# Kernel tuning notes

Measured on AMD Instinct MI355X. Metric: run time of the kernel, lower is better.

## Reference

```python
import jax, jax.numpy as jnp
import numpy as np

NT, NC, D = 20000, 80000, 256
SLOPE = 0.01  # torch F.leaky_relu default negative_slope


def _lrelu(x):
    return jnp.where(x >= 0, x, SLOPE * x)


def setup_inputs() -> dict:
    key = jax.random.key(0)
    ks = jax.random.split(key, 20)
    sc = 1.0 / np.sqrt(D)

    def W(k):
        return jax.random.normal(k, (D, D), jnp.float32) * sc

    return {
        "feat_table": jax.random.normal(ks[0], (NT, D), jnp.float32),
        "feat_column": jax.random.normal(ks[1], (NC, D), jnp.float32),
        "W_t2c": W(ks[2]), "b_t2c": jnp.zeros((D,), jnp.float32),
        "W_c2t": W(ks[3]), "b_c2t": jnp.zeros((D,), jnp.float32),
        "W_c2c": W(ks[4]), "b_c2c": jnp.zeros((D,), jnp.float32),
        "W_t2t": W(ks[5]), "b_t2t": jnp.zeros((D,), jnp.float32),
        "W_h": W(ks[6]), "b_h": jnp.zeros((D,), jnp.float32),
        "src_t2c": jax.random.randint(ks[7], (320000,), 0, NT, jnp.int32),
        "dst_t2c": jax.random.randint(ks[8], (320000,), 0, NC, jnp.int32),
        "src_c2t": jax.random.randint(ks[9], (320000,), 0, NC, jnp.int32),
        "dst_c2t": jax.random.randint(ks[10], (320000,), 0, NT, jnp.int32),
        "src_c2c": jax.random.randint(ks[11], (640000,), 0, NC, jnp.int32),
        "dst_c2c": jax.random.randint(ks[12], (640000,), 0, NC, jnp.int32),
        "src_t2t": jax.random.randint(ks[13], (160000,), 0, NT, jnp.int32),
        "dst_t2t": jax.random.randint(ks[14], (160000,), 0, NT, jnp.int32),
    }


def _mean_agg(Wh, src, dst, n_dst):
    # copy_u + mean: gather src messages, segment-mean into dst nodes
    s = jax.ops.segment_sum(Wh[src], dst, num_segments=n_dst)  # [n_dst, D]
    c = jax.ops.segment_sum(jnp.ones(src.shape, Wh.dtype), dst, num_segments=n_dst)
    return s / jnp.maximum(c, 1.0)[:, None]


def reference(feat_table, feat_column,
              W_t2c, b_t2c, W_c2t, b_c2t, W_c2c, b_c2c, W_t2t, b_t2t,
              W_h, b_h,
              src_t2c, dst_t2c, src_c2t, dst_c2t,
              src_c2c, dst_c2c, src_t2t, dst_t2t):
    # per-etype Linear + leaky_relu on source-node features
    Wh_t2c = _lrelu(feat_table @ W_t2c.T + b_t2c)
    Wh_c2t = _lrelu(feat_column @ W_c2t.T + b_c2t)
    Wh_c2c = _lrelu(feat_column @ W_c2c.T + b_c2c)
    Wh_t2t = _lrelu(feat_table @ W_t2t.T + b_t2t)

    # per-etype mean aggregation, then cross-etype 'mean' (2 etypes per ntype)
    h_table = 0.5 * (_mean_agg(Wh_c2t, src_c2t, dst_c2t, NT)
                     + _mean_agg(Wh_t2t, src_t2t, dst_t2t, NT))
    h_column = 0.5 * (_mean_agg(Wh_t2c, src_t2c, dst_t2c, NC)
                      + _mean_agg(Wh_c2c, src_c2c, dst_c2c, NC))

    out_table = _lrelu(h_table @ W_h.T + b_h) + feat_table
    out_column = _lrelu(h_column @ W_h.T + b_h) + feat_column
    return out_table, out_column
```

## Files before the change

kernel.cpp:

```cpp
#include <hip/hip_runtime.h>

#define D 256
#define SLOPE 0.01f

#define BSH 9
#define BSZ 512
#define NBMAX 160
#define EPB 8192

typedef __attribute__((ext_vector_type(8))) short bf16x8;
typedef __attribute__((ext_vector_type(4))) float f32x4;

__device__ __forceinline__ float bfbits2f(unsigned int hi) {
  return __builtin_bit_cast(float, hi);
}
__device__ __forceinline__ unsigned short f2bf(float f) {
  unsigned u = __builtin_bit_cast(unsigned, f);
  u += 0x7fffu + ((u >> 16) & 1u);
  return (unsigned short)(u >> 16);
}
__device__ __forceinline__ float lrelu(float x) {
  return (x >= 0.f) ? x : SLOPE * x;
}

__device__ __forceinline__ void gld_lds16(const void* g, void* l) {
  __builtin_amdgcn_global_load_lds(
      (const __attribute__((address_space(1))) unsigned int*)g,
      (__attribute__((address_space(3))) unsigned int*)l, 16, 0, 0);
}

__global__ void cast5_kernel(const float* w0, const float* w1, const float* w2,
                             const float* w3, const float* w4,
                             unsigned short* o0, unsigned short* o1,
                             unsigned short* o2, unsigned short* o3,
                             unsigned short* o4) {
  int a = blockIdx.y;
  const float* in = a == 0 ? w0 : a == 1 ? w1 : a == 2 ? w2 : a == 3 ? w3 : w4;
  unsigned short* out = a == 0 ? o0 : a == 1 ? o1 : a == 2 ? o2 : a == 3 ? o3 : o4;
  int i = blockIdx.x * blockDim.x + threadIdx.x;
  float4 v = ((const float4*)in)[i];
  ushort4 o;
  o.x = f2bf(v.x); o.y = f2bf(v.y); o.z = f2bf(v.z); o.w = f2bf(v.w);
  ((ushort4*)out)[i] = o;
}

__global__ __launch_bounds__(512, 1) void gemm0_dual(
    const float* __restrict__ Af, const unsigned short* __restrict__ B1,
    const unsigned short* __restrict__ B2, const float* __restrict__ bias1,
    const float* __restrict__ bias2, unsigned short* __restrict__ o1,
    unsigned short* __restrict__ o2, int M) {
  __shared__ __attribute__((aligned(16))) unsigned short Xs[64 * 256];
  const int t = threadIdx.x;
  const int wv = t >> 6, lane = t & 63;
  const int half = wv >> 2;
  const int w = wv & 3;
  const int mblk = blockIdx.x * 64;
  const int fr = lane & 15;
  const int jb = lane >> 4;

  const unsigned short* B = half ? B2 : B1;
  const float* bias = half ? bias2 : bias1;
  unsigned short* outb = half ? o2 : o1;

  float4 v0[4], v1[4];
  int cds[4];
#pragma unroll
  for (int i = 0; i < 4; i++) {
    const int c = i * 512 + t;
    const int m = c >> 5, jg = c & 31;
    int row = mblk + m;
    if (row > M - 1) row = M - 1;
    const float* gp = Af + (size_t)row * D + jg * 8;
    v0[i] = *(const float4*)gp;
    v1[i] = *(const float4*)(gp + 4);
    cds[i] = m * 32 + (jg ^ (m & 7));
  }

  bf16x8 wf[4][8];
  {
    const unsigned short* wp = B + (size_t)(w * 64 + fr) * D + jb * 8;
#pragma unroll
    for (int nt = 0; nt < 4; nt++)
#pragma unroll
      for (int k0 = 0; k0 < 8; k0++)
        wf[nt][k0] = *(const bf16x8*)(wp + nt * 16 * D + k0 * 32);
  }

#pragma unroll
  for (int i = 0; i < 4; i++) {
    uint4 pk;
    pk.x = (unsigned)f2bf(v0[i].x) | ((unsigned)f2bf(v0[i].y) << 16);
    pk.y = (unsigned)f2bf(v0[i].z) | ((unsigned)f2bf(v0[i].w) << 16);
    pk.z = (unsigned)f2bf(v1[i].x) | ((unsigned)f2bf(v1[i].y) << 16);
    pk.w = (unsigned)f2bf(v1[i].z) | ((unsigned)f2bf(v1[i].w) << 16);
    *(uint4*)&Xs[cds[i] * 8] = pk;
  }
  __syncthreads();

  f32x4 acc[4][4];
#pragma unroll
  for (int i = 0; i < 4; i++)
#pragma unroll
    for (int j = 0; j < 4; j++) acc[i][j] = (f32x4){0.f, 0.f, 0.f, 0.f};

  const int r = fr & 7;
#pragma unroll
  for (int k0 = 0; k0 < 8; k0++) {
    bf16x8 xf[4];
#pragma unroll
    for (int mt = 0; mt < 4; mt++) {
      const int ml = mt * 16 + fr;
      xf[mt] = *(const bf16x8*)&Xs[ml * 256 + (((k0 * 4 + jb) ^ r) * 8)];
    }
#pragma unroll
    for (int mt = 0; mt < 4; mt++)
#pragma unroll
      for (int nt = 0; nt < 4; nt++)
        acc[mt][nt] = __builtin_amdgcn_mfma_f32_16x16x32_bf16(
            wf[nt][k0], xf[mt], acc[mt][nt], 0, 0, 0);
  }

  const int n0 = w * 64 + jb * 4;
  float4 bv[4];
#pragma unroll
  for (int nt = 0; nt < 4; nt++) bv[nt] = *(const float4*)&bias[n0 + nt * 16];

#pragma unroll
  for (int mt = 0; mt < 4; mt++) {
    const int m = mblk + mt * 16 + fr;
    if (m < M) {
#pragma unroll
      for (int nt = 0; nt < 4; nt++) {
        ushort4 o;
        o.x = f2bf(lrelu(acc[mt][nt][0] + bv[nt].x));
        o.y = f2bf(lrelu(acc[mt][nt][1] + bv[nt].y));
        o.z = f2bf(lrelu(acc[mt][nt][2] + bv[nt].z));
        o.w = f2bf(lrelu(acc[mt][nt][3] + bv[nt].w));
        *(ushort4*)&outb[(size_t)m * D + n0 + nt * 16] = o;
      }
    }
  }
}

template <int MODE>
__global__ __launch_bounds__(256, 2) void gemm_v2(
    const unsigned short* __restrict__ A, const unsigned short* __restrict__ B,
    const float* __restrict__ bias, const float* __restrict__ residual,
    unsigned short* __restrict__ outb, float* __restrict__ outf, int M) {
  __shared__ __attribute__((aligned(16))) unsigned short Xs[64 * 256];
  const int t = threadIdx.x;
  const int w = t >> 6, lane = t & 63;
  const int mblk = blockIdx.x * 64;
  const int fr = lane & 15;
  const int jb = lane >> 4;

  bf16x8 wf[4][8];
  {
    const unsigned short* wp = B + (size_t)(w * 64 + fr) * D + jb * 8;
#pragma unroll
    for (int nt = 0; nt < 4; nt++)
#pragma unroll
      for (int k0 = 0; k0 < 8; k0++)
        wf[nt][k0] = *(const bf16x8*)(wp + nt * 16 * D + k0 * 32);
  }

#pragma unroll
  for (int i = 0; i < 8; i++) {
    const int m = (i * 4 + w) * 2 + (lane >> 5);
    int row = mblk + m;
    if (row > M - 1) row = M - 1;
    const int jsrc = (lane & 31) ^ (m & 7);
    gld_lds16(A + (size_t)row * D + jsrc * 8, &Xs[(i * 4 + w) * 512]);
  }
  asm volatile("s_waitcnt vmcnt(0)" ::: "memory");
  __syncthreads();

  f32x4 acc[4][4];
#pragma unroll
  for (int i = 0; i < 4; i++)
#pragma unroll
    for (int j = 0; j < 4; j++) acc[i][j] = (f32x4){0.f, 0.f, 0.f, 0.f};

  const int r = fr & 7;
#pragma unroll
  for (int k0 = 0; k0 < 8; k0++) {
    bf16x8 xf[4];
#pragma unroll
    for (int mt = 0; mt < 4; mt++) {
      const int ml = mt * 16 + fr;
      xf[mt] = *(const bf16x8*)&Xs[ml * 256 + (((k0 * 4 + jb) ^ r) * 8)];
    }
#pragma unroll
    for (int mt = 0; mt < 4; mt++)
#pragma unroll
      for (int nt = 0; nt < 4; nt++)
        acc[mt][nt] = __builtin_amdgcn_mfma_f32_16x16x32_bf16(
            wf[nt][k0], xf[mt], acc[mt][nt], 0, 0, 0);
  }

  const int n0 = w * 64 + jb * 4;
  float4 bv[4];
#pragma unroll
  for (int nt = 0; nt < 4; nt++) bv[nt] = *(const float4*)&bias[n0 + nt * 16];

#pragma unroll
  for (int mt = 0; mt < 4; mt++) {
    const int m = mblk + mt * 16 + fr;
    if (m < M) {
      if (MODE == 1) {
        float4 rv[4];
#pragma unroll
        for (int nt = 0; nt < 4; nt++)
          rv[nt] = *(const float4*)&residual[(size_t)m * D + n0 + nt * 16];
#pragma unroll
        for (int nt = 0; nt < 4; nt++) {
          float4 o;
          o.x = lrelu(acc[mt][nt][0] + bv[nt].x) + rv[nt].x;
          o.y = lrelu(acc[mt][nt][1] + bv[nt].y) + rv[nt].y;
          o.z = lrelu(acc[mt][nt][2] + bv[nt].z) + rv[nt].z;
          o.w = lrelu(acc[mt][nt][3] + bv[nt].w) + rv[nt].w;
          *(float4*)&outf[(size_t)m * D + n0 + nt * 16] = o;
        }
      } else {
#pragma unroll
        for (int nt = 0; nt < 4; nt++) {
          ushort4 o;
          o.x = f2bf(lrelu(acc[mt][nt][0] + bv[nt].x));
          o.y = f2bf(lrelu(acc[mt][nt][1] + bv[nt].y));
          o.z = f2bf(lrelu(acc[mt][nt][2] + bv[nt].z));
          o.w = f2bf(lrelu(acc[mt][nt][3] + bv[nt].w));
          *(ushort4*)&outb[(size_t)m * D + n0 + nt * 16] = o;
        }
      }
    }
  }
}

__global__ void hist4_kernel(const int* d0, int n0, int* c0, const int* d1,
                             int n1, int* c1, const int* d2, int n2, int* c2,
                             const int* d3, int n3, int* c3) {
  int a = blockIdx.y;
  const int* dst = a == 0 ? d0 : a == 1 ? d1 : a == 2 ? d2 : d3;
  int n = a == 0 ? n0 : a == 1 ? n1 : a == 2 ? n2 : n3;
  int* cnt = a == 0 ? c0 : a == 1 ? c1 : a == 2 ? c2 : c3;
  int i = blockIdx.x * blockDim.x + threadIdx.x;
  if (i < n) atomicAdd(&cnt[dst[i]], 1);
}

__global__ __launch_bounds__(256) void scan_p1(
    const int* c0, int n0, const int* c1, int n1, const int* c2, int n2,
    const int* c3, int n3, int* __restrict__ bsum) {
  int a = blockIdx.y;
  const int* cnt = a == 0 ? c0 : a == 1 ? c1 : a == 2 ? c2 : c3;
  int n = a == 0 ? n0 : a == 1 ? n1 : a == 2 ? n2 : n3;
  int nblk = (n + 1023) >> 10;
  int blk = blockIdx.x;
  if (blk >= nblk) return;
  int t = threadIdx.x;
  int i = (blk << 10) + t * 4;
  int s = 0;
  if (i + 3 < n) {
    int4 v = *(const int4*)(cnt + i);
    s = v.x + v.y + v.z + v.w;
  } else {
#pragma unroll
    for (int j = 0; j < 4; j++)
      if (i + j < n) s += cnt[i + j];
  }
  __shared__ int red[256];
  red[t] = s;
  __syncthreads();
  for (int off = 128; off > 0; off >>= 1) {
    if (t < off) red[t] += red[t + off];
    __syncthreads();
  }
  if (t == 0) bsum[a * 128 + blk] = red[0];
}

__global__ __launch_bounds__(128) void scan_p2(int* __restrict__ bsum, int* o0,
                                               int n0, int* o1, int n1, int* o2,
                                               int n2, int* o3, int n3) {
  int a = blockIdx.x;
  int* offs = a == 0 ? o0 : a == 1 ? o1 : a == 2 ? o2 : o3;
  int n = a == 0 ? n0 : a == 1 ? n1 : a == 2 ? n2 : n3;
  int nblk = (n + 1023) >> 10;
  int t = threadIdx.x;
  int v = (t < nblk) ? bsum[a * 128 + t] : 0;
  __shared__ int s[128];
  s[t] = v;
  __syncthreads();
  for (int off = 1; off < 128; off <<= 1) {
    int u = (t >= off) ? s[t - off] : 0;
    __syncthreads();
    s[t] += u;
    __syncthreads();
  }
  if (t < nblk) bsum[a * 128 + t] = s[t] - v;
  if (t == 127) offs[n] = s[127];
}

__global__ __launch_bounds__(256) void scan_p3(
    const int* c0, int* o0, int n0, const int* c1, int* o1, int n1,
    const int* c2, int* o2, int n2, const int* c3, int* o3, int n3,
    const int* __restrict__ bsum) {
  int a = blockIdx.y;
  const int* cnt = a == 0 ? c0 : a == 1 ? c1 : a == 2 ? c2 : c3;
  int* offs = a == 0 ? o0 : a == 1 ? o1 : a == 2 ? o2 : o3;
  int n = a == 0 ? n0 : a == 1 ? n1 : a == 2 ? n2 : n3;
  int nblk = (n + 1023) >> 10;
  int blk = blockIdx.x;
  if (blk >= nblk) return;
  int t = threadIdx.x;
  int i = (blk << 10) + t * 4;
  int4 v = {0, 0, 0, 0};
  if (i + 3 < n) {
    v = *(const int4*)(cnt + i);
  } else {
    if (i < n) v.x = cnt[i];
    if (i + 1 < n) v.y = cnt[i + 1];
    if (i + 2 < n) v.z = cnt[i + 2];
    if (i + 3 < n) v.w = cnt[i + 3];
  }
  int s = v.x + v.y + v.z + v.w;
  __shared__ int sm[256];
  sm[t] = s;
  __syncthreads();
  for (int off = 1; off < 256; off <<= 1) {
    int u = (t >= off) ? sm[t - off] : 0;
    __syncthreads();
    sm[t] += u;
    __syncthreads();
  }
  int ex = sm[t] - s + bsum[a * 128 + blk];
  int4 o;
  o.x = ex;
  o.y = ex + v.x;
  o.z = ex + v.x + v.y;
  o.w = ex + v.x + v.y + v.z;
  if (i + 3 < n) {
    *(int4*)(offs + i) = o;
  } else {
    if (i < n) offs[i] = o.x;
    if (i + 1 < n) offs[i + 1] = o.y;
    if (i + 2 < n) offs[i + 2] = o.z;
    if (i + 3 < n) offs[i + 3] = o.w;
  }
}

__global__ __launch_bounds__(256) void bucketA_kernel(
    const int* s0, const int* d0, int n0, const int* f0, int* g0, unsigned* t0, int m0,
    const int* s1, const int* d1, int n1, const int* f1, int* g1, unsigned* t1, int m1,
    const int* s2, const int* d2, int n2, const int* f2, int* g2, unsigned* t2, int m2,
    const int* s3, const int* d3, int n3, const int* f3, int* g3, unsigned* t3, int m3) {
  int a = blockIdx.y;
  const int* src = a == 0 ? s0 : a == 1 ? s1 : a == 2 ? s2 : s3;
  const int* dst = a == 0 ? d0 : a == 1 ? d1 : a == 2 ? d2 : d3;
  int n = a == 0 ? n0 : a == 1 ? n1 : a == 2 ? n2 : n3;
  const int* off = a == 0 ? f0 : a == 1 ? f1 : a == 2 ? f2 : f3;
  int* bcur = a == 0 ? g0 : a == 1 ? g1 : a == 2 ? g2 : g3;
  unsigned* temp = a == 0 ? t0 : a == 1 ? t1 : a == 2 ? t2 : t3;
  int nn = a == 0 ? m0 : a == 1 ? m1 : a == 2 ? m2 : m3;

  int blk = blockIdx.x;
  if (blk * EPB >= n) return;
  int nb = (nn + BSZ - 1) >> BSH;
  int t = threadIdx.x;
  __shared__ int cnt[NBMAX];
  __shared__ int lbase[NBMAX];
  if (t < NBMAX) cnt[t] = 0;
  __syncthreads();

  int i0 = blk * EPB + t;
#pragma unroll 4
  for (int it = 0; it < EPB / 256; it++) {
    int i = i0 + it * 256;
    if (i < n) atomicAdd(&cnt[dst[i] >> BSH], 1);
  }
  __syncthreads();
  if (t < nb) {
    int c = cnt[t];
    int g = c ? atomicAdd(&bcur[t], c) : 0;
    lbase[t] = g + off[t << BSH];
    cnt[t] = 0;
  }
  __syncthreads();
#pragma unroll 4
  for (int it = 0; it < EPB / 256; it++) {
    int i = i0 + it * 256;
    if (i < n) {
      int d = dst[i];
      int b = d >> BSH;
      int rk = atomicAdd(&cnt[b], 1);
      temp[lbase[b] + rk] = ((unsigned)src[i] << BSH) | (unsigned)(d & (BSZ - 1));
    }
  }
}

__global__ __launch_bounds__(256) void bucketB_kernel(
    const unsigned* t0, const int* f0, int* u0, int* e0, int m0,
    const unsigned* t1, const int* f1, int* u1, int* e1, int m1,
    const unsigned* t2, const int* f2, int* u2, int* e2, int m2,
    const unsigned* t3, const int* f3, int* u3, int* e3, int m3) {
  int a = blockIdx.y;
  const unsigned* temp = a == 0 ? t0 : a == 1 ? t1 : a == 2 ? t2 : t3;
  const int* off = a == 0 ? f0 : a == 1 ? f1 : a == 2 ? f2 : f3;
  int* cur = a == 0 ? u0 : a == 1 ? u1 : a == 2 ? u2 : u3;
  int* elist = a == 0 ? e0 : a == 1 ? e1 : a == 2 ? e2 : e3;
  int nn = a == 0 ? m0 : a == 1 ? m1 : a == 2 ? m2 : m3;

  int nb = (nn + BSZ - 1) >> BSH;
  int b = blockIdx.x >> 2, q = blockIdx.x & 3;
  if (b >= nb) return;
  int lo = off[b << BSH];
  int hiIdx = (b + 1) << BSH;
  if (hiIdx > nn) hiIdx = nn;
  int hi = off[hiIdx];
  int len = hi - lo;
  int chunk = (len + 3) >> 2;
  int st = lo + q * chunk;
  int en = st + chunk;
  if (en > hi) en = hi;
  for (int i = st + threadIdx.x; i < en; i += 256) {
    unsigned v = temp[i];
    int d = (b << BSH) | (int)(v & (BSZ - 1));
    int s = (int)(v >> BSH);
    int p = off[d] + atomicAdd(&cur[d], 1);
    elist[p] = s;
  }
}

__device__ __forceinline__ void add8(float* acc, uint4 p) {
  acc[0] += bfbits2f(p.x << 16);
  acc[1] += bfbits2f(p.x & 0xffff0000u);
  acc[2] += bfbits2f(p.y << 16);
  acc[3] += bfbits2f(p.y & 0xffff0000u);
  acc[4] += bfbits2f(p.z << 16);
  acc[5] += bfbits2f(p.z & 0xffff0000u);
  acc[6] += bfbits2f(p.w << 16);
  acc[7] += bfbits2f(p.w & 0xffff0000u);
}

__global__ __launch_bounds__(256) void aggregate_kernel(
    const unsigned short* __restrict__ WhA, const int* __restrict__ offsA,
    const int* __restrict__ elistA, const unsigned short* __restrict__ WhB,
    const int* __restrict__ offsB, const int* __restrict__ elistB,
    unsigned short* __restrict__ hout, int n) {
  int wave = (blockIdx.x * 256 + threadIdx.x) >> 6;
  int lane = threadIdx.x & 63;
  if (wave >= n) return;
  int half = lane >> 5;
  int l32 = lane & 31;
  size_t coff = (size_t)l32 * 8;

  float accA[8] = {0, 0, 0, 0, 0, 0, 0, 0};
  float accB[8] = {0, 0, 0, 0, 0, 0, 0, 0};
  float scA, scB;

  {
    int e0 = offsA[wave], e1 = offsA[wave + 1];
    scA = 0.5f / fmaxf((float)(e1 - e0), 1.0f);
    int e = e0;
    for (; e + 8 <= e1; e += 8) {
      int s0 = elistA[e + half];
      int s1 = elistA[e + 2 + half];
      int s2 = elistA[e + 4 + half];
      int s3 = elistA[e + 6 + half];
      uint4 p0 = *(const uint4*)(WhA + (size_t)s0 * D + coff);
      uint4 p1 = *(const uint4*)(WhA + (size_t)s1 * D + coff);
      uint4 p2 = *(const uint4*)(WhA + (size_t)s2 * D + coff);
      uint4 p3 = *(const uint4*)(WhA + (size_t)s3 * D + coff);
      add8(accA, p0); add8(accA, p1); add8(accA, p2); add8(accA, p3);
    }
    for (; e + 2 <= e1; e += 2) {
      int s0 = elistA[e + half];
      uint4 p0 = *(const uint4*)(WhA + (size_t)s0 * D + coff);
      add8(accA, p0);
    }
    if (e < e1 && half == 0) {
      int s0 = elistA[e];
      uint4 p0 = *(const uint4*)(WhA + (size_t)s0 * D + coff);
      add8(accA, p0);
    }
  }
  {
    int e0 = offsB[wave], e1 = offsB[wave + 1];
    scB = 0.5f / fmaxf((float)(e1 - e0), 1.0f);
    int e = e0;
    for (; e + 8 <= e1; e += 8) {
      int s0 = elistB[e + half];
      int s1 = elistB[e + 2 + half];
      int s2 = elistB[e + 4 + half];
      int s3 = elistB[e + 6 + half];
      uint4 p0 = *(const uint4*)(WhB + (size_t)s0 * D + coff);
      uint4 p1 = *(const uint4*)(WhB + (size_t)s1 * D + coff);
      uint4 p2 = *(const uint4*)(WhB + (size_t)s2 * D + coff);
      uint4 p3 = *(const uint4*)(WhB + (size_t)s3 * D + coff);
      add8(accB, p0); add8(accB, p1); add8(accB, p2); add8(accB, p3);
    }
    for (; e + 2 <= e1; e += 2) {
      int s0 = elistB[e + half];
      uint4 p0 = *(const uint4*)(WhB + (size_t)s0 * D + coff);
      add8(accB, p0);
    }
    if (e < e1 && half == 0) {
      int s0 = elistB[e];
      uint4 p0 = *(const uint4*)(WhB + (size_t)s0 * D + coff);
      add8(accB, p0);
    }
  }

  float h[8];
#pragma unroll
  for (int j = 0; j < 8; j++) {
    h[j] = accA[j] * scA + accB[j] * scB;
    h[j] += __shfl_down(h[j], 32);
  }
  if (half == 0) {
    uint4 o;
    o.x = (unsigned)f2bf(h[0]) | ((unsigned)f2bf(h[1]) << 16);
    o.y = (unsigned)f2bf(h[2]) | ((unsigned)f2bf(h[3]) << 16);
    o.z = (unsigned)f2bf(h[4]) | ((unsigned)f2bf(h[5]) << 16);
    o.w = (unsigned)f2bf(h[6]) | ((unsigned)f2bf(h[7]) << 16);
    *(uint4*)(hout + (size_t)wave * D + coff) = o;
  }
}

extern "C" void kernel_launch(void* const* d_in, const int* in_sizes, int n_in,
                              void* d_out, int out_size, void* d_ws,
                              size_t ws_size, hipStream_t stream) {
  const float* feat_table = (const float*)d_in[0];
  const float* feat_column = (const float*)d_in[1];
  const float* Wsrc[5] = {(const float*)d_in[2], (const float*)d_in[4],
                          (const float*)d_in[6], (const float*)d_in[8],
                          (const float*)d_in[10]};
  const float* b_t2c = (const float*)d_in[3];
  const float* b_c2t = (const float*)d_in[5];
  const float* b_c2c = (const float*)d_in[7];
  const float* b_t2t = (const float*)d_in[9];
  const float* b_h = (const float*)d_in[11];
  const int* src_t2c = (const int*)d_in[12];
  const int* dst_t2c = (const int*)d_in[13];
  const int* src_c2t = (const int*)d_in[14];
  const int* dst_c2t = (const int*)d_in[15];
  const int* src_c2c = (const int*)d_in[16];
  const int* dst_c2c = (const int*)d_in[17];
  const int* src_t2t = (const int*)d_in[18];
  const int* dst_t2t = (const int*)d_in[19];

  const int NT = in_sizes[0] / D;
  const int NC = in_sizes[1] / D;
  const int E_t2c = in_sizes[12], E_c2t = in_sizes[14];
  const int E_c2c = in_sizes[16], E_t2t = in_sizes[18];

  char* ws = (char*)d_ws;
  size_t cur = 0;
  auto alloc = [&](size_t bytes) -> void* {
    void* p = ws + cur;
    cur += (bytes + 255) & ~(size_t)255;
    return p;
  };
  unsigned short* Wb[5];
  for (int i = 0; i < 5; i++) Wb[i] = (unsigned short*)alloc((size_t)D * D * 2);
  unsigned short* Wh_t2c = (unsigned short*)alloc((size_t)NT * D * 2);
  unsigned short* Wh_c2t = (unsigned short*)alloc((size_t)NC * D * 2);
  unsigned short* Wh_c2c = (unsigned short*)alloc((size_t)NC * D * 2);
  unsigned short* Wh_t2t = (unsigned short*)alloc((size_t)NT * D * 2);
  unsigned short* h_tab = (unsigned short*)alloc((size_t)NT * D * 2);
  unsigned short* h_col = (unsigned short*)alloc((size_t)NC * D * 2);
  size_t nints = 2 * (2 * (size_t)NT + 2 * (size_t)NC) + 4 * NBMAX;
  int* ints = (int*)alloc(sizeof(int) * nints);
  int* cnt_c2t = ints;
  int* cnt_t2t = cnt_c2t + NT;
  int* cnt_t2c = cnt_t2t + NT;
  int* cnt_c2c = cnt_t2c + NC;
  int* cur_c2t = cnt_c2c + NC;
  int* cur_t2t = cur_c2t + NT;
  int* cur_t2c = cur_t2t + NT;
  int* cur_c2c = cur_t2c + NC;
  int* bc_c2t = cur_c2c + NC;
  int* bc_t2t = bc_c2t + NBMAX;
  int* bc_t2c = bc_t2t + NBMAX;
  int* bc_c2c = bc_t2c + NBMAX;
  int* off_c2t = (int*)alloc(sizeof(int) * (NT + 1));
  int* off_t2t = (int*)alloc(sizeof(int) * (NT + 1));
  int* off_t2c = (int*)alloc(sizeof(int) * (NC + 1));
  int* off_c2c = (int*)alloc(sizeof(int) * (NC + 1));
  int* el_c2t = (int*)alloc(sizeof(int) * E_c2t);
  int* el_t2t = (int*)alloc(sizeof(int) * E_t2t);
  int* el_t2c = (int*)alloc(sizeof(int) * E_t2c);
  int* el_c2c = (int*)alloc(sizeof(int) * E_c2c);
  unsigned* tp_c2t = (unsigned*)alloc(sizeof(unsigned) * E_c2t);
  unsigned* tp_t2t = (unsigned*)alloc(sizeof(unsigned) * E_t2t);
  unsigned* tp_t2c = (unsigned*)alloc(sizeof(unsigned) * E_t2c);
  unsigned* tp_c2c = (unsigned*)alloc(sizeof(unsigned) * E_c2c);
  int* bsum = (int*)alloc(sizeof(int) * 4 * 128);

  hipMemsetAsync(ints, 0, sizeof(int) * nints, stream);

  {
    dim3 g((D * D / 4 + 255) / 256, 5);
    cast5_kernel<<<g, 256, 0, stream>>>(Wsrc[0], Wsrc[1], Wsrc[2], Wsrc[3],
                                        Wsrc[4], Wb[0], Wb[1], Wb[2], Wb[3],
                                        Wb[4]);
  }

  gemm0_dual<<<(NT + 63) / 64, 512, 0, stream>>>(
      feat_table, Wb[0], Wb[3], b_t2c, b_t2t, Wh_t2c, Wh_t2t, NT);
  gemm0_dual<<<(NC + 63) / 64, 512, 0, stream>>>(
      feat_column, Wb[1], Wb[2], b_c2t, b_c2c, Wh_c2t, Wh_c2c, NC);

  int Emax = max(max(E_c2t, E_t2t), max(E_t2c, E_c2c));
  {
    dim3 g((Emax + 255) / 256, 4);
    hist4_kernel<<<g, 256, 0, stream>>>(dst_c2t, E_c2t, cnt_c2t, dst_t2t,
                                        E_t2t, cnt_t2t, dst_t2c, E_t2c,
                                        cnt_t2c, dst_c2c, E_c2c, cnt_c2c);
  }
  int nmax = max(NT, NC);
  {
    dim3 g((nmax + 1023) / 1024, 4);
    scan_p1<<<g, 256, 0, stream>>>(cnt_c2t, NT, cnt_t2t, NT, cnt_t2c, NC,
                                   cnt_c2c, NC, bsum);
    scan_p2<<<4, 128, 0, stream>>>(bsum, off_c2t, NT, off_t2t, NT, off_t2c, NC,
                                   off_c2c, NC);
    scan_p3<<<g, 256, 0, stream>>>(cnt_c2t, off_c2t, NT, cnt_t2t, off_t2t, NT,
                                   cnt_t2c, off_t2c, NC, cnt_c2c, off_c2c, NC,
                                   bsum);
  }
  {
    dim3 g((Emax + EPB - 1) / EPB, 4);
    bucketA_kernel<<<g, 256, 0, stream>>>(
        src_c2t, dst_c2t, E_c2t, off_c2t, bc_c2t, tp_c2t, NT,
        src_t2t, dst_t2t, E_t2t, off_t2t, bc_t2t, tp_t2t, NT,
        src_t2c, dst_t2c, E_t2c, off_t2c, bc_t2c, tp_t2c, NC,
        src_c2c, dst_c2c, E_c2c, off_c2c, bc_c2c, tp_c2c, NC);
  }
  {
    int nbmax = (max(NT, NC) + BSZ - 1) >> BSH;
    dim3 g(nbmax * 4, 4);
    bucketB_kernel<<<g, 256, 0, stream>>>(
        tp_c2t, off_c2t, cur_c2t, el_c2t, NT,
        tp_t2t, off_t2t, cur_t2t, el_t2t, NT,
        tp_t2c, off_t2c, cur_t2c, el_t2c, NC,
        tp_c2c, off_c2c, cur_c2c, el_c2c, NC);
  }

  aggregate_kernel<<<(NT + 3) / 4, 256, 0, stream>>>(
      Wh_c2t, off_c2t, el_c2t, Wh_t2t, off_t2t, el_t2t, h_tab, NT);
  aggregate_kernel<<<(NC + 3) / 4, 256, 0, stream>>>(
      Wh_t2c, off_t2c, el_t2c, Wh_c2c, off_c2c, el_c2c, h_col, NC);

  float* out_tab = (float*)d_out;
  float* out_col = out_tab + (size_t)NT * D;
  gemm_v2<1><<<(NT + 63) / 64, 256, 0, stream>>>(h_tab, Wb[4], b_h, feat_table,
                                                 nullptr, out_tab, NT);
  gemm_v2<1><<<(NC + 63) / 64, 256, 0, stream>>>(h_col, Wb[4], b_h, feat_column,
                                                 nullptr, out_col, NC);
}
```

Before: 616.6 us.

## Pre-cast features to bf16, merge per-etype GEMMs and aggregations into batched launches

Adds a standalone cast of the fp32 node features to bf16 so that all four first-layer GEMMs can run in one 4-way grid using the shared bf16 gemm core, replacing the two dual-GEMM kernels that cast inline. The two aggregation launches and the two output GEMM launches are each merged into a single 2D-grid launch, which cuts launch count and tail effects. The bf16 feature buffers are then reused as scratch for the bucket temp pairs and the aggregated h outputs to save memory. In exchange, the extra cast pass writes and re-reads the features, and the merged grids carry blocks that exit early for the smaller node type.

Measured after the change: 611.5 us. No clear change (-0.8%).

```diff
diff --git a/kernel.cpp b/kernel.cpp
--- a/kernel.cpp
+++ b/kernel.cpp
@@ -27,6 +27,16 @@
   __builtin_amdgcn_global_load_lds(
       (const __attribute__((address_space(1))) unsigned int*)g,
       (__attribute__((address_space(3))) unsigned int*)l, 16, 0, 0);
+}
+
+__global__ void cast_kernel(const float* __restrict__ in,
+                            unsigned short* __restrict__ out, int n4) {
+  int i = blockIdx.x * blockDim.x + threadIdx.x;
+  if (i >= n4) return;
+  float4 v = ((const float4*)in)[i];
+  ushort4 o;
+  o.x = f2bf(v.x); o.y = f2bf(v.y); o.z = f2bf(v.z); o.w = f2bf(v.w);
+  ((ushort4*)out)[i] = o;
 }
 
 __global__ void cast5_kernel(const float* w0, const float* w1, const float* w2,
@@ -44,113 +54,14 @@
   ((ushort4*)out)[i] = o;
 }
 
-__global__ __launch_bounds__(512, 1) void gemm0_dual(
-    const float* __restrict__ Af, const unsigned short* __restrict__ B1,
-    const unsigned short* __restrict__ B2, const float* __restrict__ bias1,
-    const float* __restrict__ bias2, unsigned short* __restrict__ o1,
-    unsigned short* __restrict__ o2, int M) {
-  __shared__ __attribute__((aligned(16))) unsigned short Xs[64 * 256];
-  const int t = threadIdx.x;
-  const int wv = t >> 6, lane = t & 63;
-  const int half = wv >> 2;
-  const int w = wv & 3;
-  const int mblk = blockIdx.x * 64;
-  const int fr = lane & 15;
-  const int jb = lane >> 4;
-
-  const unsigned short* B = half ? B2 : B1;
-  const float* bias = half ? bias2 : bias1;
-  unsigned short* outb = half ? o2 : o1;
-
-  float4 v0[4], v1[4];
-  int cds[4];
-#pragma unroll
-  for (int i = 0; i < 4; i++) {
-    const int c = i * 512 + t;
-    const int m = c >> 5, jg = c & 31;
-    int row = mblk + m;
-    if (row > M - 1) row = M - 1;
-    const float* gp = Af + (size_t)row * D + jg * 8;
-    v0[i] = *(const float4*)gp;
-    v1[i] = *(const float4*)(gp + 4);
-    cds[i] = m * 32 + (jg ^ (m & 7));
-  }
-
-  bf16x8 wf[4][8];
-  {
-    const unsigned short* wp = B + (size_t)(w * 64 + fr) * D + jb * 8;
-#pragma unroll
-    for (int nt = 0; nt < 4; nt++)
-#pragma unroll
-      for (int k0 = 0; k0 < 8; k0++)
-        wf[nt][k0] = *(const bf16x8*)(wp + nt * 16 * D + k0 * 32);
-  }
-
-#pragma unroll
-  for (int i = 0; i < 4; i++) {
-    uint4 pk;
-    pk.x = (unsigned)f2bf(v0[i].x) | ((unsigned)f2bf(v0[i].y) << 16);
-    pk.y = (unsigned)f2bf(v0[i].z) | ((unsigned)f2bf(v0[i].w) << 16);
-    pk.z = (unsigned)f2bf(v1[i].x) | ((unsigned)f2bf(v1[i].y) << 16);
-    pk.w = (unsigned)f2bf(v1[i].z) | ((unsigned)f2bf(v1[i].w) << 16);
-    *(uint4*)&Xs[cds[i] * 8] = pk;
-  }
-  __syncthreads();
-
-  f32x4 acc[4][4];
-#pragma unroll
-  for (int i = 0; i < 4; i++)
-#pragma unroll
-    for (int j = 0; j < 4; j++) acc[i][j] = (f32x4){0.f, 0.f, 0.f, 0.f};
-
-  const int r = fr & 7;
-#pragma unroll
-  for (int k0 = 0; k0 < 8; k0++) {
-    bf16x8 xf[4];
-#pragma unroll
-    for (int mt = 0; mt < 4; mt++) {
-      const int ml = mt * 16 + fr;
-      xf[mt] = *(const bf16x8*)&Xs[ml * 256 + (((k0 * 4 + jb) ^ r) * 8)];
-    }
-#pragma unroll
-    for (int mt = 0; mt < 4; mt++)
-#pragma unroll
-      for (int nt = 0; nt < 4; nt++)
-        acc[mt][nt] = __builtin_amdgcn_mfma_f32_16x16x32_bf16(
-            wf[nt][k0], xf[mt], acc[mt][nt], 0, 0, 0);
-  }
-
-  const int n0 = w * 64 + jb * 4;
-  float4 bv[4];
-#pragma unroll
-  for (int nt = 0; nt < 4; nt++) bv[nt] = *(const float4*)&bias[n0 + nt * 16];
-
-#pragma unroll
-  for (int mt = 0; mt < 4; mt++) {
-    const int m = mblk + mt * 16 + fr;
-    if (m < M) {
-#pragma unroll
-      for (int nt = 0; nt < 4; nt++) {
-        ushort4 o;
-        o.x = f2bf(lrelu(acc[mt][nt][0] + bv[nt].x));
-        o.y = f2bf(lrelu(acc[mt][nt][1] + bv[nt].y));
-        o.z = f2bf(lrelu(acc[mt][nt][2] + bv[nt].z));
-        o.w = f2bf(lrelu(acc[mt][nt][3] + bv[nt].w));
-        *(ushort4*)&outb[(size_t)m * D + n0 + nt * 16] = o;
-      }
-    }
-  }
-}
-
 template <int MODE>
-__global__ __launch_bounds__(256, 2) void gemm_v2(
-    const unsigned short* __restrict__ A, const unsigned short* __restrict__ B,
-    const float* __restrict__ bias, const float* __restrict__ residual,
-    unsigned short* __restrict__ outb, float* __restrict__ outf, int M) {
-  __shared__ __attribute__((aligned(16))) unsigned short Xs[64 * 256];
+__device__ __forceinline__ void gemm_core(
+    unsigned short* Xs, const unsigned short* __restrict__ A,
+    const unsigned short* __restrict__ B, const float* __restrict__ bias,
+    const float* __restrict__ residual, unsigned short* __restrict__ outb,
+    float* __restrict__ outf, int M, int mblk) {
   const int t = threadIdx.x;
   const int w = t >> 6, lane = t & 63;
-  const int mblk = blockIdx.x * 64;
   const int fr = lane & 15;
   const int jb = lane >> 4;
 
@@ -234,6 +145,39 @@
       }
     }
   }
+}
+
+__global__ __launch_bounds__(256, 2) void gemm0_quad(
+    const unsigned short* __restrict__ A0, const unsigned short* __restrict__ A1,
+    const unsigned short* __restrict__ B0, const unsigned short* __restrict__ B1,
+    const unsigned short* __restrict__ B2, const unsigned short* __restrict__ B3,
+    const float* b0, const float* b1, const float* b2, const float* b3,
+    unsigned short* o0, unsigned short* o1, unsigned short* o2,
+    unsigned short* o3, int M0, int M1) {
+  __shared__ __attribute__((aligned(16))) unsigned short Xs[64 * 256];
+  int a = blockIdx.y;
+  const unsigned short* A = (a < 2) ? A0 : A1;
+  int M = (a < 2) ? M0 : M1;
+  int mblk = blockIdx.x * 64;
+  if (mblk >= M) return;
+  const unsigned short* B = a == 0 ? B0 : a == 1 ? B1 : a == 2 ? B2 : B3;
+  const float* bias = a == 0 ? b0 : a == 1 ? b1 : a == 2 ? b2 : b3;
+  unsigned short* outb = a == 0 ? o0 : a == 1 ? o1 : a == 2 ? o2 : o3;
+  gemm_core<0>(Xs, A, B, bias, nullptr, outb, nullptr, M, mblk);
+}
+
+__global__ __launch_bounds__(256, 2) void gemm1_dual(
+    const unsigned short* __restrict__ A0, const unsigned short* __restrict__ A1,
+    const unsigned short* __restrict__ Bw, const float* bh,
+    const float* __restrict__ r0, const float* __restrict__ r1,
+    float* __restrict__ o0, float* __restrict__ o1, int M0, int M1) {
+  __shared__ __attribute__((aligned(16))) unsigned short Xs[64 * 256];
+  int a = blockIdx.y;
+  const unsigned short* A = a ? A1 : A0;
+  int M = a ? M1 : M0;
+  int mblk = blockIdx.x * 64;
+  if (mblk >= M) return;
+  gemm_core<1>(Xs, A, Bw, bh, a ? r1 : r0, nullptr, a ? o1 : o0, M, mblk);
 }
 
 __global__ void hist4_kernel(const int* d0, int n0, int* c0, const int* d1,
@@ -440,14 +384,11 @@
   acc[7] += bfbits2f(p.w & 0xffff0000u);
 }
 
-__global__ __launch_bounds__(256) void aggregate_kernel(
+__device__ __forceinline__ void agg_core(
     const unsigned short* __restrict__ WhA, const int* __restrict__ offsA,
     const int* __restrict__ elistA, const unsigned short* __restrict__ WhB,
     const int* __restrict__ offsB, const int* __restrict__ elistB,
-    unsigned short* __restrict__ hout, int n) {
-  int wave = (blockIdx.x * 256 + threadIdx.x) >> 6;
-  int lane = threadIdx.x & 63;
-  if (wave >= n) return;
+    unsigned short* __restrict__ hout, int n, int wave, int lane) {
   int half = lane >> 5;
   int l32 = lane & 31;
   size_t coff = (size_t)l32 * 8;
@@ -523,6 +464,24 @@
     o.w = (unsigned)f2bf(h[6]) | ((unsigned)f2bf(h[7]) << 16);
     *(uint4*)(hout + (size_t)wave * D + coff) = o;
   }
+}
+
+__global__ __launch_bounds__(256) void aggregate2_kernel(
+    const unsigned short* WhA0, const int* offsA0, const int* elA0,
+    const unsigned short* WhB0, const int* offsB0, const int* elB0,
+    unsigned short* h0, int n0,
+    const unsigned short* WhA1, const int* offsA1, const int* elA1,
+    const unsigned short* WhB1, const int* offsB1, const int* elB1,
+    unsigned short* h1, int n1) {
+  int a = blockIdx.y;
+  int n = a ? n1 : n0;
+  int wave = (blockIdx.x * 256 + threadIdx.x) >> 6;
+  int lane = threadIdx.x & 63;
+  if (wave >= n) return;
+  if (a == 0)
+    agg_core(WhA0, offsA0, elA0, WhB0, offsB0, elB0, h0, n0, wave, lane);
+  else
+    agg_core(WhA1, offsA1, elA1, WhB1, offsB1, elB1, h1, n1, wave, lane);
 }
 
 extern "C" void kernel_launch(void* const* d_in, const int* in_sizes, int n_in,
@@ -561,12 +520,12 @@
   };
   unsigned short* Wb[5];
   for (int i = 0; i < 5; i++) Wb[i] = (unsigned short*)alloc((size_t)D * D * 2);
+  unsigned short* ftb = (unsigned short*)alloc((size_t)NT * D * 2);
+  unsigned short* fcb = (unsigned short*)alloc((size_t)NC * D * 2);
   unsigned short* Wh_t2c = (unsigned short*)alloc((size_t)NT * D * 2);
   unsigned short* Wh_c2t = (unsigned short*)alloc((size_t)NC * D * 2);
   unsigned short* Wh_c2c = (unsigned short*)alloc((size_t)NC * D * 2);
   unsigned short* Wh_t2t = (unsigned short*)alloc((size_t)NT * D * 2);
-  unsigned short* h_tab = (unsigned short*)alloc((size_t)NT * D * 2);
-  unsigned short* h_col = (unsigned short*)alloc((size_t)NC * D * 2);
   size_t nints = 2 * (2 * (size_t)NT + 2 * (size_t)NC) + 4 * NBMAX;
   int* ints = (int*)alloc(sizeof(int) * nints);
   int* cnt_c2t = ints;
@@ -589,11 +548,14 @@
   int* el_t2t = (int*)alloc(sizeof(int) * E_t2t);
   int* el_t2c = (int*)alloc(sizeof(int) * E_t2c);
   int* el_c2c = (int*)alloc(sizeof(int) * E_c2c);
-  unsigned* tp_c2t = (unsigned*)alloc(sizeof(unsigned) * E_c2t);
-  unsigned* tp_t2t = (unsigned*)alloc(sizeof(unsigned) * E_t2t);
-  unsigned* tp_t2c = (unsigned*)alloc(sizeof(unsigned) * E_t2c);
-  unsigned* tp_c2c = (unsigned*)alloc(sizeof(unsigned) * E_c2c);
   int* bsum = (int*)alloc(sizeof(int) * 4 * 128);
+
+  unsigned* tp_c2t = (unsigned*)ftb;
+  unsigned* tp_t2t = tp_c2t + E_c2t;
+  unsigned* tp_t2c = tp_t2t + E_t2t;
+  unsigned* tp_c2c = tp_t2c + E_t2c;
+  unsigned short* h_tab = ftb;
+  unsigned short* h_col = fcb;
 
   hipMemsetAsync(ints, 0, sizeof(int) * nints, stream);
 
@@ -603,11 +565,17 @@
                                         Wsrc[4], Wb[0], Wb[1], Wb[2], Wb[3],
                                         Wb[4]);
   }
-
-  gemm0_dual<<<(NT + 63) / 64, 512, 0, stream>>>(
-      feat_table, Wb[0], Wb[3], b_t2c, b_t2t, Wh_t2c, Wh_t2t, NT);
-  gemm0_dual<<<(NC + 63) / 64, 512, 0, stream>>>(
-      feat_column, Wb[1], Wb[2], b_c2t, b_c2c, Wh_c2t, Wh_c2c, NC);
+  cast_kernel<<<((NT * D / 4) + 255) / 256, 256, 0, stream>>>(feat_table, ftb,
+                                                              NT * D / 4);
+  cast_kernel<<<((NC * D / 4) + 255) / 256, 256, 0, stream>>>(feat_column, fcb,
+                                                              NC * D / 4);
+
+  {
+    dim3 g((max(NT, NC) + 63) / 64, 4);
+    gemm0_quad<<<g, 256, 0, stream>>>(ftb, fcb, Wb[0], Wb[3], Wb[1], Wb[2],
+                                      b_t2c, b_t2t, b_c2t, b_c2c, Wh_t2c,
+                                      Wh_t2t, Wh_c2t, Wh_c2c, NT, NC);
+  }
 
   int Emax = max(max(E_c2t, E_t2t), max(E_t2c, E_c2c));
   {
@@ -645,15 +613,18 @@
         tp_c2c, off_c2c, cur_c2c, el_c2c, NC);
   }
 
-  aggregate_kernel<<<(NT + 3) / 4, 256, 0, stream>>>(
-      Wh_c2t, off_c2t, el_c2t, Wh_t2t, off_t2t, el_t2t, h_tab, NT);
-  aggregate_kernel<<<(NC + 3) / 4, 256, 0, stream>>>(
-      Wh_t2c, off_t2c, el_t2c, Wh_c2c, off_c2c, el_c2c, h_col, NC);
+  {
+    dim3 g((max(NT, NC) + 3) / 4, 2);
+    aggregate2_kernel<<<g, 256, 0, stream>>>(
+        Wh_c2t, off_c2t, el_c2t, Wh_t2t, off_t2t, el_t2t, h_tab, NT,
+        Wh_t2c, off_t2c, el_t2c, Wh_c2c, off_c2c, el_c2c, h_col, NC);
+  }
 
   float* out_tab = (float*)d_out;
   float* out_col = out_tab + (size_t)NT * D;
-  gemm_v2<1><<<(NT + 63) / 64, 256, 0, stream>>>(h_tab, Wb[4], b_h, feat_table,
-                                                 nullptr, out_tab, NT);
-  gemm_v2<1><<<(NC + 63) / 64, 256, 0, stream>>>(h_col, Wb[4], b_h, feat_column,
-                                                 nullptr, out_col, NC);
-}
+  {
+    dim3 g((max(NT, NC) + 63) / 64, 2);
+    gemm1_dual<<<g, 256, 0, stream>>>(h_tab, h_col, Wb[4], b_h, feat_table,
+                                      feat_column, out_tab, out_col, NT, NC);
+  }
+}
```
